# Kernel tuning notes

Hardware: AMD Instinct MI355X
Metric: run time of the kernel (lower is better)

## Reference

```python
import jax, jax.numpy as jnp
import numpy as np

EPS = 1e-5
GROUPS = 32


def group_norm(x, gamma, beta):
    # x: [b, c, h, w]
    b, c, h, w = x.shape
    xg = x.reshape(b, GROUPS, c // GROUPS, h, w)
    mu = jnp.mean(xg, axis=(2, 3, 4), keepdims=True)
    var = jnp.var(xg, axis=(2, 3, 4), keepdims=True)
    xg = (xg - mu) / jnp.sqrt(var + EPS)
    x = xg.reshape(b, c, h, w)
    return x * gamma[None, :, None, None] + beta[None, :, None, None]


def conv1x1(x, w, bias):
    # x: [b, c_in, h, w], w: [c_out, c_in] -> [b, c_out, h, w]
    return jnp.einsum('oc,bchw->bohw', w, x) + bias[None, :, None, None]


def setup_inputs() -> dict:
    key = jax.random.key(0)
    ks = jax.random.split(key, 6)
    c = 512
    s = 1.0 / np.sqrt(c)
    x = jax.random.normal(ks[0], (8, c, 64, 64), dtype=jnp.float32)
    return {
        'x': x,
        'gn_gamma': jnp.ones((c,), jnp.float32),
        'gn_beta': jnp.zeros((c,), jnp.float32),
        'wq': jax.random.normal(ks[1], (c, c), jnp.float32) * s,
        'bq': jnp.zeros((c,), jnp.float32),
        'wk': jax.random.normal(ks[2], (c, c), jnp.float32) * s,
        'bk': jnp.zeros((c,), jnp.float32),
        'wv': jax.random.normal(ks[3], (c, c), jnp.float32) * s,
        'bv': jnp.zeros((c,), jnp.float32),
        'wo': jax.random.normal(ks[4], (c, c), jnp.float32) * s,
        'bo': jnp.zeros((c,), jnp.float32),
    }


def reference(x, gn_gamma, gn_beta, wq, bq, wk, bk, wv, bv, wo, bo):
    b, c, h, w = x.shape
    hidden = group_norm(x, gn_gamma, gn_beta)
    q = conv1x1(hidden, wq, bq).reshape(b, c, h * w).transpose(0, 2, 1)  # [b, hw, c]
    k = conv1x1(hidden, wk, bk).reshape(b, c, h * w)                      # [b, c, hw]
    v = conv1x1(hidden, wv, bv).reshape(b, c, h * w).transpose(0, 2, 1)  # [b, hw, c]
    # NOTE: faithful to source — attention logits are MULTIPLIED by sqrt(c)
    attn = jnp.einsum('bqc,bck->bqk', q, k) * jnp.float32(c) ** 0.5
    attn = jax.nn.softmax(attn, axis=-1)
    attn_h = jnp.einsum('bqk,bkc->bqc', attn, v)                          # [b, hw, c]
    attn_h = attn_h.transpose(0, 2, 1).reshape(b, c, h, w)
    return x + conv1x1(attn_h, wo, bo)
```

## Files before the change

kernel.cpp:

```cpp
#include <hip/hip_runtime.h>
#include <stdint.h>

typedef unsigned short u16;
typedef unsigned int u32;
typedef __attribute__((ext_vector_type(4))) float f32x4;
typedef __attribute__((ext_vector_type(8))) __bf16 bf16x8;
typedef __attribute__((ext_vector_type(4))) unsigned short u16x4;

#define DEVINL __device__ __forceinline__

DEVINL u16 f2bf(float f) {
  u32 u = __builtin_bit_cast(u32, f);
  u32 r = (u + 0x7fffu + ((u >> 16) & 1u)) >> 16;
  return (u16)r;
}
DEVINL float bf2f(u16 h) {
  u32 u = ((u32)h) << 16;
  return __builtin_bit_cast(float, u);
}

DEVINL f32x4 mfma16(bf16x8 a, bf16x8 b, f32x4 c) {
  return __builtin_amdgcn_mfma_f32_16x16x32_bf16(a, b, c, 0, 0, 0);
}

DEVINL void gload_lds16(const void* g, void* l) {
  auto gp = (__attribute__((address_space(1))) void*)(reinterpret_cast<uintptr_t>(g));
  auto lp = (__attribute__((address_space(3))) void*)(u32)(reinterpret_cast<uintptr_t>(l));
  __builtin_amdgcn_global_load_lds(gp, lp, 16, 0, 0);
}

template <int ROWS, int KCS, int NT>
DEVINL void stage_tile(const u16* __restrict__ g, int ld, char* lds, int tid) {
  constexpr int SWZ = (KCS - 1) < 7 ? (KCS - 1) : 7;
  constexpr int CH = ROWS * KCS;
#pragma unroll
  for (int c0 = 0; c0 < CH; c0 += NT) {
    int c = c0 + tid;
    int row = c / KCS;
    int slot = c & (KCS - 1);
    const u16* src = g + (size_t)row * ld + ((slot ^ (row & SWZ)) << 3);
    char* dst = lds + (((size_t)(c0 + (tid & ~63))) << 4);
    gload_lds16(src, dst);
  }
}

template <int KCS, int SWZM>
DEVINL bf16x8 fragk(const char* lds, int row, int kslot) {
  return *reinterpret_cast<const bf16x8*>(
      lds + (size_t)row * (KCS * 16) + (size_t)((kslot ^ (row & SWZM)) << 4));
}

__global__ __launch_bounds__(256) void gn_stats(const float* __restrict__ x,
                                                float* __restrict__ smean,
                                                float* __restrict__ srstd) {
  const int bg = blockIdx.x;
  const float4* base = reinterpret_cast<const float4*>(x + (size_t)bg * 65536);
  float s = 0.f, ss = 0.f;
  for (int i = threadIdx.x; i < 16384; i += 256) {
    float4 v = base[i];
    s += v.x + v.y + v.z + v.w;
    ss += v.x * v.x + v.y * v.y + v.z * v.z + v.w * v.w;
  }
#pragma unroll
  for (int off = 1; off < 64; off <<= 1) {
    s += __shfl_xor(s, off);
    ss += __shfl_xor(ss, off);
  }
  __shared__ float rs_[4], rss_[4];
  int w = threadIdx.x >> 6;
  if ((threadIdx.x & 63) == 0) { rs_[w] = s; rss_[w] = ss; }
  __syncthreads();
  if (threadIdx.x == 0) {
    float S = rs_[0] + rs_[1] + rs_[2] + rs_[3];
    float SS = rss_[0] + rss_[1] + rss_[2] + rss_[3];
    float mu = S * (1.0f / 65536.0f);
    float var = SS * (1.0f / 65536.0f) - mu * mu;
    smean[bg] = mu;
    srstd[bg] = 1.0f / sqrtf(var + 1e-5f);
  }
}

__global__ __launch_bounds__(256) void gn_apply(
    const float* __restrict__ x, const float* __restrict__ gamma,
    const float* __restrict__ beta, const float* __restrict__ smean,
    const float* __restrict__ srstd, u16* __restrict__ hhi, u16* __restrict__ hlo) {
  __shared__ __align__(16) u16 thi[128][136];
  __shared__ __align__(16) u16 tlo[128][136];
  const int b = blockIdx.z, p0 = blockIdx.y * 128, c0 = blockIdx.x * 128;
  const int tid = threadIdx.x;
  const int ci = tid >> 1, ph = tid & 1;
  const int c = c0 + ci;
  const int bg = b * 32 + (c >> 4);
  const float mu = smean[bg], rstd = srstd[bg];
  const float ga = gamma[c] * rstd;
  const float be = beta[c] - mu * ga;
  const float* xrow = x + ((size_t)(b * 512 + c)) * 4096 + p0;
#pragma unroll
  for (int s = 0; s < 16; s++) {
    int pj = ph * 4 + s * 8;
    float4 v = *reinterpret_cast<const float4*>(xrow + pj);
    float h0 = v.x * ga + be, h1 = v.y * ga + be, h2 = v.z * ga + be, h3 = v.w * ga + be;
    u16 a0 = f2bf(h0), a1 = f2bf(h1), a2 = f2bf(h2), a3 = f2bf(h3);
    thi[pj + 0][ci] = a0; tlo[pj + 0][ci] = f2bf(h0 - bf2f(a0));
    thi[pj + 1][ci] = a1; tlo[pj + 1][ci] = f2bf(h1 - bf2f(a1));
    thi[pj + 2][ci] = a2; tlo[pj + 2][ci] = f2bf(h2 - bf2f(a2));
    thi[pj + 3][ci] = a3; tlo[pj + 3][ci] = f2bf(h3 - bf2f(a3));
  }
  __syncthreads();
  u16* oh = hhi + ((size_t)b * 4096 + p0) * 512 + c0;
  u16* ol = hlo + ((size_t)b * 4096 + p0) * 512 + c0;
  for (int cc = tid; cc < 2048; cc += 256) {
    int p = cc >> 4, sli = cc & 15;
    *reinterpret_cast<bf16x8*>(oh + (size_t)p * 512 + sli * 8) =
        *reinterpret_cast<const bf16x8*>(&thi[p][sli * 8]);
    *reinterpret_cast<bf16x8*>(ol + (size_t)p * 512 + sli * 8) =
        *reinterpret_cast<const bf16x8*>(&tlo[p][sli * 8]);
  }
}

__global__ __launch_bounds__(256) void prep_w(
    const float* __restrict__ wq, const float* __restrict__ wk,
    const float* __restrict__ wv, const float* __restrict__ wo,
    u16* __restrict__ wqh, u16* __restrict__ wql, u16* __restrict__ wkh,
    u16* __restrict__ wkl, u16* __restrict__ wvb, u16* __restrict__ wob) {
  int i = blockIdx.x * 256 + threadIdx.x;
  if (i >= 262144) return;
  float a = wq[i]; u16 h = f2bf(a); wqh[i] = h; wql[i] = f2bf(a - bf2f(h));
  float bb = wk[i]; h = f2bf(bb); wkh[i] = h; wkl[i] = f2bf(bb - bf2f(h));
  wvb[i] = f2bf(wv[i]);
  wob[i] = f2bf(wo[i]);
}

template <int MODE>
__global__ __launch_bounds__(256, 2) void conv_gemm(
    const u16* __restrict__ A0, const u16* __restrict__ A1,
    const u16* __restrict__ B0, const u16* __restrict__ B1,
    const float* __restrict__ bias, const float* __restrict__ xres,
    u16* __restrict__ o0, u16* __restrict__ o1, float* __restrict__ of,
    long sAb, long sBb) {
  constexpr int LDSZ = (MODE == 0) ? 65536 : ((MODE == 1) ? 34816 : 32768);
  __shared__ __align__(16) char lds[LDSZ];
  char* ldsA = lds;
  char* ldsB = lds + 16384;

  const int b = blockIdx.z;
  const int n0 = blockIdx.x * 128;
  const int m0 = blockIdx.y * 128;
  const int tid = threadIdx.x;
  const int lane = tid & 63;
  const int w = tid >> 6;
  const int li = lane & 15, gq = lane >> 4;
  const int wm = (w >> 1) * 64, wn = (w & 1) * 64;

  const u16* Ag = A0 + (size_t)b * sAb + (size_t)m0 * 512;
  const u16* Bg = B0 + (size_t)b * sBb + (size_t)n0 * 512;
  const u16* Ag1 = (MODE == 0) ? (A1 + (size_t)b * sAb + (size_t)m0 * 512) : nullptr;
  const u16* Bg1 = (MODE == 0) ? (B1 + (size_t)b * sBb + (size_t)n0 * 512) : nullptr;

  f32x4 acc[4][4] = {};

  for (int k0 = 0; k0 < 512; k0 += 64) {
    __syncthreads();
    stage_tile<128, 8, 256>(Ag + k0, 512, ldsA, tid);
    stage_tile<128, 8, 256>(Bg + k0, 512, ldsB, tid);
    if (MODE == 0) {
      stage_tile<128, 8, 256>(Ag1 + k0, 512, lds + 32768, tid);
      stage_tile<128, 8, 256>(Bg1 + k0, 512, lds + 49152, tid);
    }
    __syncthreads();
#pragma unroll
    for (int kk = 0; kk < 2; kk++) {
      bf16x8 aF[4], bF[4], aL[4], bL[4];
#pragma unroll
      for (int t = 0; t < 4; t++) {
        aF[t] = fragk<8, 7>(ldsA, wm + t * 16 + li, kk * 4 + gq);
        bF[t] = fragk<8, 7>(ldsB, wn + t * 16 + li, kk * 4 + gq);
        if (MODE == 0) {
          aL[t] = fragk<8, 7>(lds + 32768, wm + t * 16 + li, kk * 4 + gq);
          bL[t] = fragk<8, 7>(lds + 49152, wn + t * 16 + li, kk * 4 + gq);
        }
      }
#pragma unroll
      for (int mt = 0; mt < 4; mt++)
#pragma unroll
        for (int nt = 0; nt < 4; nt++) {
          acc[mt][nt] = mfma16(aF[mt], bF[nt], acc[mt][nt]);
          if (MODE == 0) {
            acc[mt][nt] = mfma16(aF[mt], bL[nt], acc[mt][nt]);
            acc[mt][nt] = mfma16(aL[mt], bF[nt], acc[mt][nt]);
          }
        }
    }
  }

  if (MODE == 0) {
#pragma unroll
    for (int nt = 0; nt < 4; nt++) {
      int gn = n0 + wn + nt * 16 + li;
      float bs = bias[gn];
#pragma unroll
      for (int mt = 0; mt < 4; mt++)
#pragma unroll
        for (int r = 0; r < 4; r++) {
          int gm = m0 + wm + mt * 16 + gq * 4 + r;
          float v = acc[mt][nt][r] + bs;
          u16 hi = f2bf(v);
          size_t idx = ((size_t)b * 4096 + gm) * 512 + gn;
          o0[idx] = hi;
          o1[idx] = f2bf(v - bf2f(hi));
        }
    }
  } else if (MODE == 1) {
    __syncthreads();
    u16* vt = (u16*)lds;
#pragma unroll
    for (int nt = 0; nt < 4; nt++) {
      int ol = wn + nt * 16 + li;
      float bs = bias[n0 + ol];
#pragma unroll
      for (int mt = 0; mt < 4; mt++)
#pragma unroll
        for (int r = 0; r < 4; r++) {
          int pl = wm + mt * 16 + gq * 4 + r;
          vt[ol * 136 + pl] = f2bf(acc[mt][nt][r] + bs);
        }
    }
    __syncthreads();
    for (int c = tid; c < 2048; c += 256) {
      int o = c >> 4, sl = c & 15;
      bf16x8 val = *reinterpret_cast<const bf16x8*>(vt + o * 136 + sl * 8);
      *reinterpret_cast<bf16x8*>(o0 + ((size_t)b * 512 + n0 + o) * 4096 + m0 + sl * 8) = val;
    }
  } else {
#pragma unroll
    for (int nt = 0; nt < 4; nt++) {
      int gn = n0 + wn + nt * 16 + li;
#pragma unroll
      for (int mt = 0; mt < 4; mt++)
#pragma unroll
        for (int r = 0; r < 4; r++) {
          int gm = m0 + wm + mt * 16 + gq * 4 + r;
          size_t idx = ((size_t)b * 512 + gm) * 4096 + gn;
          of[idx] = acc[mt][nt][r] + bias[gm] + xres[idx];
        }
    }
  }
}

#define S2C 32.64446259f

__global__ __launch_bounds__(512) void flash_attn(
    const u16* __restrict__ qhi, const u16* __restrict__ qlo,
    const u16* __restrict__ khi, const u16* __restrict__ klo,
    const u16* __restrict__ vbuf, u16* __restrict__ oout) {
  __shared__ __align__(16) char ldsK[65536];
  __shared__ float sm[64], sl[64], srs[64];
  __shared__ float pmax[2][64], psum[2][64];

  const int bid = blockIdx.x;
  const int b = bid & 7, qt = bid >> 3;
  const int i0 = qt * 64;
  const int tid = threadIdx.x;
  const int lane = tid & 63, w = tid >> 6;
  const int li = lane & 15, gq = lane >> 4;
  const int mt_qk = w >> 1, jh = w & 1;
  const int wc = w * 64;

  if (tid < 64) { sm[tid] = -3.0e38f; sl[tid] = 0.0f; }

  const u16* Kh = khi + (size_t)b * 4096 * 512;
  const u16* Kl = klo + (size_t)b * 4096 * 512;
  const u16* qbh = qhi + ((size_t)(b * 4096 + i0 + mt_qk * 16 + li)) * 512 + gq * 8;
  const u16* qbl = qlo + ((size_t)(b * 4096 + i0 + mt_qk * 16 + li)) * 512 + gq * 8;
  const u16* Vb = vbuf + (size_t)b * 512 * 4096;
  u16* Pl = (u16*)(ldsK + 32768);

  stage_tile<128, 8, 512>(Kh, 512, ldsK, tid);
  stage_tile<128, 8, 512>(Kl, 512, ldsK + 16384, tid);

  f32x4 Oa[4][4] = {};

  for (int j0 = 0; j0 < 4096; j0 += 128) {
    f32x4 lg[4] = {};
#pragma unroll
    for (int cc = 0; cc < 8; cc++) {
      const int c0 = cc * 64;
      const char* cur = ldsK + (size_t)(cc & 1) * 32768;
      __syncthreads();
      if (cc < 7) {
        char* nxt = ldsK + (size_t)((cc + 1) & 1) * 32768;
        stage_tile<128, 8, 512>(Kh + (size_t)j0 * 512 + c0 + 64, 512, nxt, tid);
        stage_tile<128, 8, 512>(Kl + (size_t)j0 * 512 + c0 + 64, 512, nxt + 16384, tid);
      }
#pragma unroll
      for (int kk = 0; kk < 2; kk++) {
        bf16x8 qhf = *reinterpret_cast<const bf16x8*>(qbh + c0 + kk * 32);
        bf16x8 qlf = *reinterpret_cast<const bf16x8*>(qbl + c0 + kk * 32);
        __builtin_amdgcn_s_setprio(1);
#pragma unroll
        for (int nt = 0; nt < 4; nt++) {
          int krow = jh * 64 + nt * 16 + li;
          bf16x8 bh = fragk<8, 7>(cur, krow, kk * 4 + gq);
          bf16x8 bl = fragk<8, 7>(cur + 16384, krow, kk * 4 + gq);
          lg[nt] = mfma16(bh, qhf, lg[nt]);
          lg[nt] = mfma16(bl, qhf, lg[nt]);
          lg[nt] = mfma16(bh, qlf, lg[nt]);
        }
        __builtin_amdgcn_s_setprio(0);
      }
    }
    bf16x8 vA[4], vB[4];
#pragma unroll
    for (int t = 0; t < 4; t++)
      vA[t] = *reinterpret_cast<const bf16x8*>(
          Vb + (size_t)(wc + t * 16 + li) * 4096 + j0 + gq * 8);
#pragma unroll
    for (int t = 0; t < 4; t++)
      vB[t] = *reinterpret_cast<const bf16x8*>(
          Vb + (size_t)(wc + t * 16 + li) * 4096 + j0 + 32 + gq * 8);
    const int i_ = mt_qk * 16 + li;
    {
      float mx = lg[0][0];
#pragma unroll
      for (int nt = 0; nt < 4; nt++)
#pragma unroll
        for (int r = 0; r < 4; r++) mx = fmaxf(mx, lg[nt][r]);
      mx = fmaxf(mx, __shfl_xor(mx, 16));
      mx = fmaxf(mx, __shfl_xor(mx, 32));
      if (lane < 16) pmax[jh][i_] = mx;
    }
    __syncthreads();
    if (tid < 64) {
      float tm = fmaxf(pmax[0][tid], pmax[1][tid]);
      float mo = sm[tid];
      float mn = fmaxf(mo, tm);
      float rs = exp2f(S2C * (mo - mn));
      sm[tid] = mn; srs[tid] = rs; sl[tid] *= rs;
    }
    __syncthreads();
    {
      float mn = sm[i_];
      float ps = 0.0f;
#pragma unroll
      for (int nt = 0; nt < 4; nt++) {
        float p0 = exp2f(S2C * (lg[nt][0] - mn));
        float p1 = exp2f(S2C * (lg[nt][1] - mn));
        float p2 = exp2f(S2C * (lg[nt][2] - mn));
        float p3 = exp2f(S2C * (lg[nt][3] - mn));
        ps += (p0 + p1) + (p2 + p3);
        u16x4 pk = {f2bf(p0), f2bf(p1), f2bf(p2), f2bf(p3)};
        int jb = jh * 64 + nt * 16 + gq * 4;
        char* dst = (char*)Pl + (size_t)i_ * 256 +
                    (((jb >> 3) ^ (i_ & 15)) << 4) + ((jb << 1) & 15);
        *reinterpret_cast<u16x4*>(dst) = pk;
      }
      ps += __shfl_xor(ps, 16);
      ps += __shfl_xor(ps, 32);
      if (lane < 16) psum[jh][i_] = ps;
    }
    __syncthreads();
    if (tid < 64) sl[tid] += psum[0][tid] + psum[1][tid];
    if (j0 + 128 < 4096) {
      stage_tile<128, 8, 512>(Kh + (size_t)(j0 + 128) * 512, 512, ldsK, tid);
      stage_tile<128, 8, 512>(Kl + (size_t)(j0 + 128) * 512, 512, ldsK + 16384, tid);
    }
#pragma unroll
    for (int mt = 0; mt < 4; mt++)
#pragma unroll
      for (int r = 0; r < 4; r++) {
        float rr = srs[mt * 16 + gq * 4 + r];
#pragma unroll
        for (int nt = 0; nt < 4; nt++) Oa[mt][nt][r] *= rr;
      }
#define PVSTEP(JJ, VREG)                                                      \
    {                                                                         \
      __builtin_amdgcn_s_setprio(1);                                          \
      _Pragma("unroll")                                                       \
      for (int mt = 0; mt < 4; mt++) {                                        \
        bf16x8 pa = fragk<16, 15>((const char*)Pl, mt * 16 + li, (JJ) * 4 + gq); \
        _Pragma("unroll")                                                     \
        for (int nt = 0; nt < 4; nt++)                                        \
          Oa[mt][nt] = mfma16(pa, VREG[nt], Oa[mt][nt]);                      \
      }                                                                       \
      __builtin_amdgcn_s_setprio(0);                                          \
    }
    PVSTEP(0, vA)
#pragma unroll
    for (int t = 0; t < 4; t++)
      vA[t] = *reinterpret_cast<const bf16x8*>(
          Vb + (size_t)(wc + t * 16 + li) * 4096 + j0 + 64 + gq * 8);
    PVSTEP(1, vB)
#pragma unroll
    for (int t = 0; t < 4; t++)
      vB[t] = *reinterpret_cast<const bf16x8*>(
          Vb + (size_t)(wc + t * 16 + li) * 4096 + j0 + 96 + gq * 8);
    PVSTEP(2, vA)
    PVSTEP(3, vB)
#undef PVSTEP
  }

  __syncthreads();
#pragma unroll
  for (int mt = 0; mt < 4; mt++)
#pragma unroll
    for (int r = 0; r < 4; r++) {
      int i2 = mt * 16 + gq * 4 + r;
      float inv = 1.0f / sl[i2];
#pragma unroll
      for (int nt = 0; nt < 4; nt++) {
        float o = Oa[mt][nt][r] * inv;
        oout[((size_t)(b * 4096 + i0 + i2)) * 512 + wc + nt * 16 + li] = f2bf(o);
      }
    }
}

extern "C" void kernel_launch(void* const* d_in, const int* in_sizes, int n_in,
                              void* d_out, int out_size, void* d_ws, size_t ws_size,
                              hipStream_t stream) {
  const float* x = (const float*)d_in[0];
  const float* gamma = (const float*)d_in[1];
  const float* beta = (const float*)d_in[2];
  const float* wq = (const float*)d_in[3];
  const float* bq = (const float*)d_in[4];
  const float* wk = (const float*)d_in[5];
  const float* bk = (const float*)d_in[6];
  const float* wv = (const float*)d_in[7];
  const float* bv = (const float*)d_in[8];
  const float* wo = (const float*)d_in[9];
  const float* bo = (const float*)d_in[10];

  char* ws = (char*)d_ws;
  const size_t SZ = (size_t)8 * 4096 * 512 * 2;
  const size_t NEED = 7 * SZ + 6 * (size_t)524288 + 2048;
  if (ws_size < NEED) return;

  u16* hhi = (u16*)(ws);
  u16* hlo = (u16*)(ws + SZ);
  u16* qhi = (u16*)(ws + 2 * SZ);
  u16* qlo = (u16*)(ws + 3 * SZ);
  u16* khi = (u16*)(ws + 4 * SZ);
  u16* klo = (u16*)(ws + 5 * SZ);
  u16* vbf = (u16*)(ws + 6 * SZ);
  u16* ah  = qhi;
  u16* wqh = (u16*)(ws + 7 * SZ);
  u16* wql = wqh + 262144;
  u16* wkh = wql + 262144;
  u16* wkl = wkh + 262144;
  u16* wvb = wkl + 262144;
  u16* wob = wvb + 262144;
  float* smean = (float*)(wob + 262144);
  float* srstd = smean + 256;

  prep_w<<<1024, 256, 0, stream>>>(wq, wk, wv, wo, wqh, wql, wkh, wkl, wvb, wob);
  gn_stats<<<256, 256, 0, stream>>>(x, smean, srstd);
  gn_apply<<<dim3(4, 32, 8), 256, 0, stream>>>(x, gamma, beta, smean, srstd, hhi, hlo);
  conv_gemm<0><<<dim3(4, 32, 8), 256, 0, stream>>>(hhi, hlo, wqh, wql, bq, nullptr,
                                                   qhi, qlo, nullptr, (long)4096 * 512, 0);
  conv_gemm<0><<<dim3(4, 32, 8), 256, 0, stream>>>(hhi, hlo, wkh, wkl, bk, nullptr,
                                                   khi, klo, nullptr, (long)4096 * 512, 0);
  conv_gemm<1><<<dim3(4, 32, 8), 256, 0, stream>>>(hhi, nullptr, wvb, nullptr, bv, nullptr,
                                                   vbf, nullptr, nullptr, (long)4096 * 512, 0);
  flash_attn<<<512, 512, 0, stream>>>(qhi, qlo, khi, klo, vbf, ah);
  conv_gemm<2><<<dim3(32, 4, 8), 256, 0, stream>>>(wob, nullptr, ah, nullptr, bo, x,
                                                   nullptr, nullptr, (float*)d_out,
                                                   0, (long)4096 * 512);
}
```

Measured before the change: 1.235 ms.

## Process 256 keys per softmax step with a separate P buffer and continuous K prefetch

The flash attention loop now handles two 128-key sub-tiles per outer iteration, cutting the number of softmax/rescale rounds and their barriers in half. P gets its own 32KB LDS buffer, so the K double-buffer prefetch can run continuously across sub-tiles and outer iterations instead of being restaged after softmax. The per-row max/rescale bookkeeping is computed redundantly by each wave, which removes one __syncthreads. The cost is more LDS (96KB+), which may limit occupancy, and more accumulator registers (lg0/lg1).

```diff
diff --git a/kernel.cpp b/kernel.cpp
--- a/kernel.cpp
+++ b/kernel.cpp
@@ -254,6 +254,7 @@
     const u16* __restrict__ khi, const u16* __restrict__ klo,
     const u16* __restrict__ vbuf, u16* __restrict__ oout) {
   __shared__ __align__(16) char ldsK[65536];
+  __shared__ __align__(16) char ldsP[32768];
   __shared__ float sm[64], sl[64], srs[64];
   __shared__ float pmax[2][64], psum[2][64];
 
@@ -273,40 +274,51 @@
   const u16* qbh = qhi + ((size_t)(b * 4096 + i0 + mt_qk * 16 + li)) * 512 + gq * 8;
   const u16* qbl = qlo + ((size_t)(b * 4096 + i0 + mt_qk * 16 + li)) * 512 + gq * 8;
   const u16* Vb = vbuf + (size_t)b * 512 * 4096;
-  u16* Pl = (u16*)(ldsK + 32768);
 
   stage_tile<128, 8, 512>(Kh, 512, ldsK, tid);
   stage_tile<128, 8, 512>(Kl, 512, ldsK + 16384, tid);
 
   f32x4 Oa[4][4] = {};
 
-  for (int j0 = 0; j0 < 4096; j0 += 128) {
-    f32x4 lg[4] = {};
-#pragma unroll
-    for (int cc = 0; cc < 8; cc++) {
-      const int c0 = cc * 64;
-      const char* cur = ldsK + (size_t)(cc & 1) * 32768;
-      __syncthreads();
-      if (cc < 7) {
-        char* nxt = ldsK + (size_t)((cc + 1) & 1) * 32768;
-        stage_tile<128, 8, 512>(Kh + (size_t)j0 * 512 + c0 + 64, 512, nxt, tid);
-        stage_tile<128, 8, 512>(Kl + (size_t)j0 * 512 + c0 + 64, 512, nxt + 16384, tid);
-      }
-#pragma unroll
-      for (int kk = 0; kk < 2; kk++) {
-        bf16x8 qhf = *reinterpret_cast<const bf16x8*>(qbh + c0 + kk * 32);
-        bf16x8 qlf = *reinterpret_cast<const bf16x8*>(qbl + c0 + kk * 32);
-        __builtin_amdgcn_s_setprio(1);
-#pragma unroll
-        for (int nt = 0; nt < 4; nt++) {
-          int krow = jh * 64 + nt * 16 + li;
-          bf16x8 bh = fragk<8, 7>(cur, krow, kk * 4 + gq);
-          bf16x8 bl = fragk<8, 7>(cur + 16384, krow, kk * 4 + gq);
-          lg[nt] = mfma16(bh, qhf, lg[nt]);
-          lg[nt] = mfma16(bl, qhf, lg[nt]);
-          lg[nt] = mfma16(bh, qlf, lg[nt]);
-        }
-        __builtin_amdgcn_s_setprio(0);
+  for (int j0 = 0; j0 < 4096; j0 += 256) {
+    f32x4 lg0[4] = {}, lg1[4] = {};
+#pragma unroll
+    for (int js = 0; js < 2; js++) {
+      const size_t jrow = (size_t)(j0 + js * 128) * 512;
+#pragma unroll
+      for (int cc = 0; cc < 8; cc++) {
+        const int c0 = cc * 64;
+        const int n = js * 8 + cc;
+        const char* cur = ldsK + (size_t)(n & 1) * 32768;
+        __syncthreads();
+        {
+          const int np = n + 1;
+          const int pj = j0 + (np >> 3) * 128;
+          if (pj < 4096) {
+            char* nxt = ldsK + (size_t)(np & 1) * 32768;
+            stage_tile<128, 8, 512>(Kh + (size_t)pj * 512 + (np & 7) * 64, 512, nxt, tid);
+            stage_tile<128, 8, 512>(Kl + (size_t)pj * 512 + (np & 7) * 64, 512,
+                                    nxt + 16384, tid);
+          }
+        }
+#pragma unroll
+        for (int kk = 0; kk < 2; kk++) {
+          bf16x8 qhf = *reinterpret_cast<const bf16x8*>(qbh + c0 + kk * 32);
+          bf16x8 qlf = *reinterpret_cast<const bf16x8*>(qbl + c0 + kk * 32);
+          __builtin_amdgcn_s_setprio(1);
+#pragma unroll
+          for (int nt = 0; nt < 4; nt++) {
+            int krow = jh * 64 + nt * 16 + li;
+            bf16x8 bh = fragk<8, 7>(cur, krow, kk * 4 + gq);
+            bf16x8 bl = fragk<8, 7>(cur + 16384, krow, kk * 4 + gq);
+            f32x4 acc = js ? lg1[nt] : lg0[nt];
+            acc = mfma16(bh, qhf, acc);
+            acc = mfma16(bl, qhf, acc);
+            acc = mfma16(bh, qlf, acc);
+            if (js) lg1[nt] = acc; else lg0[nt] = acc;
+          }
+          __builtin_amdgcn_s_setprio(0);
+        }
       }
     }
     bf16x8 vA[4], vB[4];
@@ -320,49 +332,50 @@
           Vb + (size_t)(wc + t * 16 + li) * 4096 + j0 + 32 + gq * 8);
     const int i_ = mt_qk * 16 + li;
     {
-      float mx = lg[0][0];
+      float mx = lg0[0][0];
 #pragma unroll
       for (int nt = 0; nt < 4; nt++)
 #pragma unroll
-        for (int r = 0; r < 4; r++) mx = fmaxf(mx, lg[nt][r]);
+        for (int r = 0; r < 4; r++) {
+          mx = fmaxf(mx, lg0[nt][r]);
+          mx = fmaxf(mx, lg1[nt][r]);
+        }
       mx = fmaxf(mx, __shfl_xor(mx, 16));
       mx = fmaxf(mx, __shfl_xor(mx, 32));
       if (lane < 16) pmax[jh][i_] = mx;
     }
     __syncthreads();
-    if (tid < 64) {
-      float tm = fmaxf(pmax[0][tid], pmax[1][tid]);
-      float mo = sm[tid];
-      float mn = fmaxf(mo, tm);
-      float rs = exp2f(S2C * (mo - mn));
-      sm[tid] = mn; srs[tid] = rs; sl[tid] *= rs;
-    }
-    __syncthreads();
+    const float mo = sm[i_];
+    const float mn = fmaxf(mo, fmaxf(pmax[0][i_], pmax[1][i_]));
+    if (jh == 0 && lane < 16) srs[i_] = exp2f(S2C * (mo - mn));
     {
-      float mn = sm[i_];
       float ps = 0.0f;
 #pragma unroll
-      for (int nt = 0; nt < 4; nt++) {
-        float p0 = exp2f(S2C * (lg[nt][0] - mn));
-        float p1 = exp2f(S2C * (lg[nt][1] - mn));
-        float p2 = exp2f(S2C * (lg[nt][2] - mn));
-        float p3 = exp2f(S2C * (lg[nt][3] - mn));
-        ps += (p0 + p1) + (p2 + p3);
-        u16x4 pk = {f2bf(p0), f2bf(p1), f2bf(p2), f2bf(p3)};
-        int jb = jh * 64 + nt * 16 + gq * 4;
-        char* dst = (char*)Pl + (size_t)i_ * 256 +
-                    (((jb >> 3) ^ (i_ & 15)) << 4) + ((jb << 1) & 15);
-        *reinterpret_cast<u16x4*>(dst) = pk;
+      for (int js = 0; js < 2; js++) {
+        char* Pt = ldsP + (size_t)js * 16384;
+#pragma unroll
+        for (int nt = 0; nt < 4; nt++) {
+          f32x4 lgv = js ? lg1[nt] : lg0[nt];
+          float p0 = exp2f(S2C * (lgv[0] - mn));
+          float p1 = exp2f(S2C * (lgv[1] - mn));
+          float p2 = exp2f(S2C * (lgv[2] - mn));
+          float p3 = exp2f(S2C * (lgv[3] - mn));
+          ps += (p0 + p1) + (p2 + p3);
+          u16x4 pk = {f2bf(p0), f2bf(p1), f2bf(p2), f2bf(p3)};
+          int jb = jh * 64 + nt * 16 + gq * 4;
+          char* dst = Pt + (size_t)i_ * 256 +
+                      (((jb >> 3) ^ (i_ & 15)) << 4) + ((jb << 1) & 15);
+          *reinterpret_cast<u16x4*>(dst) = pk;
+        }
       }
       ps += __shfl_xor(ps, 16);
       ps += __shfl_xor(ps, 32);
       if (lane < 16) psum[jh][i_] = ps;
     }
     __syncthreads();
-    if (tid < 64) sl[tid] += psum[0][tid] + psum[1][tid];
-    if (j0 + 128 < 4096) {
-      stage_tile<128, 8, 512>(Kh + (size_t)(j0 + 128) * 512, 512, ldsK, tid);
-      stage_tile<128, 8, 512>(Kl + (size_t)(j0 + 128) * 512, 512, ldsK + 16384, tid);
+    if (jh == 0 && lane < 16) {
+      sl[i_] = sl[i_] * srs[i_] + psum[0][i_] + psum[1][i_];
+      sm[i_] = mn;
     }
 #pragma unroll
     for (int mt = 0; mt < 4; mt++)
@@ -374,29 +387,32 @@
       }
 #define PVSTEP(JJ, VREG)                                                      \
     {                                                                         \
+      const char* Pt = ldsP + (size_t)((JJ) >> 2) * 16384;                    \
       __builtin_amdgcn_s_setprio(1);                                          \
       _Pragma("unroll")                                                       \
       for (int mt = 0; mt < 4; mt++) {                                        \
-        bf16x8 pa = fragk<16, 15>((const char*)Pl, mt * 16 + li, (JJ) * 4 + gq); \
+        bf16x8 pa = fragk<16, 15>(Pt, mt * 16 + li, ((JJ) & 3) * 4 + gq);     \
         _Pragma("unroll")                                                     \
         for (int nt = 0; nt < 4; nt++)                                        \
           Oa[mt][nt] = mfma16(pa, VREG[nt], Oa[mt][nt]);                      \
       }                                                                       \
       __builtin_amdgcn_s_setprio(0);                                          \
     }
-    PVSTEP(0, vA)
-#pragma unroll
-    for (int t = 0; t < 4; t++)
-      vA[t] = *reinterpret_cast<const bf16x8*>(
-          Vb + (size_t)(wc + t * 16 + li) * 4096 + j0 + 64 + gq * 8);
-    PVSTEP(1, vB)
-#pragma unroll
-    for (int t = 0; t < 4; t++)
-      vB[t] = *reinterpret_cast<const bf16x8*>(
-          Vb + (size_t)(wc + t * 16 + li) * 4096 + j0 + 96 + gq * 8);
-    PVSTEP(2, vA)
-    PVSTEP(3, vB)
+#define VLOAD(VREG, OFF)                                                      \
+    _Pragma("unroll")                                                         \
+    for (int t = 0; t < 4; t++)                                               \
+      VREG[t] = *reinterpret_cast<const bf16x8*>(                             \
+          Vb + (size_t)(wc + t * 16 + li) * 4096 + j0 + (OFF) + gq * 8);
+    PVSTEP(0, vA) VLOAD(vA, 64)
+    PVSTEP(1, vB) VLOAD(vB, 96)
+    PVSTEP(2, vA) VLOAD(vA, 128)
+    PVSTEP(3, vB) VLOAD(vB, 160)
+    PVSTEP(4, vA) VLOAD(vA, 192)
+    PVSTEP(5, vB) VLOAD(vB, 224)
+    PVSTEP(6, vA)
+    PVSTEP(7, vB)
 #undef PVSTEP
+#undef VLOAD
   }
 
   __syncthreads();
```

After: 1.226 ms. No clear change (-0.7%).
